# Performance work log

Measured on AMD Instinct MI355X. Metric: run time of the kernel, lower is better.

The kernel has to match this reference:

```python
import jax, jax.numpy as jnp
import numpy as np

B, T, DIM, S, DFF = 4, 2048, 2048, 4, 8192
SINKHORN_ITERS = 10


def setup_inputs() -> dict:
    key = jax.random.key(0)
    ks = jax.random.split(key, 12)

    def lin(k, fan_in, shape):
        bound = 1.0 / np.sqrt(fan_in)
        return jax.random.uniform(k, shape, jnp.float32, -bound, bound)

    return {
        "x": jax.random.normal(ks[0], (B, T, DIM), jnp.float32),
        # phi_* linears act on the S-times tiled vector of size S*DIM
        "phi_pre_w": lin(ks[1], S * DIM, (S, S * DIM)),
        "phi_pre_b": lin(ks[2], S * DIM, (S,)),
        "phi_post_w": lin(ks[3], S * DIM, (S, S * DIM)),
        "phi_post_b": lin(ks[4], S * DIM, (S,)),
        "phi_res_w": lin(ks[5], S * DIM, (S * S, S * DIM)),
        "phi_res_b": lin(ks[6], S * DIM, (S * S,)),
        "alpha_pre": jnp.ones((1,), jnp.float32),
        "alpha_post": jnp.ones((1,), jnp.float32),
        "alpha_res": jnp.ones((1,), jnp.float32),
        "b_pre": jnp.zeros((S,), jnp.float32),
        "b_post": jnp.zeros((S,), jnp.float32),
        "b_res": jnp.zeros((S, S), jnp.float32),
        # block = transformer MLP
        "W1": lin(ks[7], DIM, (DIM, DFF)),
        "b1": lin(ks[8], DIM, (DFF,)),
        "W2": lin(ks[9], DFF, (DFF, DIM)),
        "b2": lin(ks[10], DFF, (DIM,)),
    }


def sinkhorn_knopp(logits):
    # logits: [B, T, S, S] -> doubly-stochastic via exp + alternating normalization
    M = jnp.exp(logits)
    for _ in range(SINKHORN_ITERS):
        M = M / jnp.sum(M, axis=-1, keepdims=True)  # rows
        M = M / jnp.sum(M, axis=-2, keepdims=True)  # cols
    return M


def reference(x, phi_pre_w, phi_pre_b, phi_post_w, phi_post_b, phi_res_w,
              phi_res_b, alpha_pre, alpha_post, alpha_res, b_pre, b_post,
              b_res, W1, b1, W2, b2):
    bs, seq, d = x.shape
    s = b_pre.shape[0]
    eps = jnp.asarray(jnp.finfo(x.dtype).eps, x.dtype)
    # x_l = x expanded over S identical streams; x_vec = tile(x, S).
    # RMS over the tiled S*d vector == RMS over d (streams are copies).
    x_n = x * jax.lax.rsqrt(jnp.mean(x * x, axis=-1, keepdims=True) + eps)
    # Linear on the tiled vector == sum of the S weight blocks applied to x_n.
    Wp = phi_pre_w.reshape(s, s, d).sum(axis=1)        # [S, d]
    Wq = phi_post_w.reshape(s, s, d).sum(axis=1)       # [S, d]
    Wr = phi_res_w.reshape(s * s, s, d).sum(axis=1)    # [S*S, d]
    h_pre_t = alpha_pre * (jnp.einsum('btd,sd->bts', x_n, Wp) + phi_pre_b) + b_pre
    h_post_t = alpha_post * (jnp.einsum('btd,sd->bts', x_n, Wq) + phi_post_b) + b_post
    h_res_t = alpha_res * (jnp.einsum('btd,kd->btk', x_n, Wr) + phi_res_b)
    h_res_t = h_res_t.reshape(bs, seq, s, s) + b_res
    h_pre = jax.nn.sigmoid(h_pre_t)                    # [B,T,S]
    h_post = 2.0 * jax.nn.sigmoid(h_post_t)            # [B,T,S]
    h_res = sinkhorn_knopp(h_res_t)                    # [B,T,S,S]
    # block_input = sum_j x_l[:,:,j] * h_pre[...,j] ; streams identical -> x * sum_j h_pre
    block_input = x * jnp.sum(h_pre, axis=-1, keepdims=True)
    # block: MLP with exact (erf) GELU, matching torch default
    h = jax.nn.gelu(jnp.einsum('btd,df->btf', block_input, W1) + b1, approximate=False)
    block_out = jnp.einsum('btf,fd->btd', h, W2) + b2
    # out = sum_i [ (h_res @ x_l)_i + h_post_i * block_out ]
    #     = x * sum_{ij} h_res[ij] + block_out * sum_i h_post_i
    res_mix = jnp.sum(h_res, axis=(-2, -1))[..., None]         # [B,T,1]
    post_mix = jnp.sum(h_post, axis=-1, keepdims=True)          # [B,T,1]
    return x * res_mix + block_out * post_mix
```

## Files before the change

kernel.cpp:

```cpp
#include <hip/hip_runtime.h>
#include <hip/hip_bf16.h>
#include <cstdint>
#include <cstddef>

#define DIM   2048
#define DFF   8192
#define NROWS 8192
#define NFOLD 24

typedef float f32x4 __attribute__((ext_vector_type(4)));
typedef __bf16 bf16x8 __attribute__((ext_vector_type(8)));

__device__ __forceinline__ float sigmoidf_(float v) { return 1.0f / (1.0f + expf(-v)); }

__device__ __forceinline__ unsigned short f2bf(float v) {
    union { __hip_bfloat16 h; unsigned short u; } cv;
    cv.h = __float2bfloat16(v);
    return cv.u;
}

__device__ __forceinline__ void async_copy16(const void* g, void* l) {
    __builtin_amdgcn_global_load_lds((const __attribute__((address_space(1))) void*)g,
                                     (__attribute__((address_space(3))) void*)l, 16, 0, 0);
}

__device__ __forceinline__ void wg_barrier() {
    asm volatile("" ::: "memory");
    __builtin_amdgcn_s_barrier();
    asm volatile("" ::: "memory");
}

#define VM(n)  asm volatile("s_waitcnt vmcnt(" #n ")" ::: "memory")
#define LGKM0  asm volatile("s_waitcnt lgkmcnt(0)" ::: "memory")

__global__ __launch_bounds__(256) void fold_kernel(const float* __restrict__ pre_w,
                                                   const float* __restrict__ post_w,
                                                   const float* __restrict__ res_w,
                                                   float* __restrict__ Wfold) {
    int idx = blockIdx.x * 256 + threadIdx.x;
    if (idx >= NFOLD * DIM) return;
    int r = idx >> 11;
    int d = idx & (DIM - 1);
    const float* src;
    if (r < 4)      src = pre_w  + (size_t)r * (4 * DIM);
    else if (r < 8) src = post_w + (size_t)(r - 4) * (4 * DIM);
    else            src = res_w  + (size_t)(r - 8) * (4 * DIM);
    Wfold[idx] = src[d] + src[DIM + d] + src[2 * DIM + d] + src[3 * DIM + d];
}

__global__ __launch_bounds__(256) void transpose_to_bf16(const float* __restrict__ in,
                                                         __hip_bfloat16* __restrict__ out,
                                                         int R, int C) {
    __shared__ float tile[32][33];
    const int bx = blockIdx.x, by = blockIdx.y;
    const int t = threadIdx.x;
    const int lr = t >> 3;
    const int lc = (t & 7) * 4;

    float4 v = *(const float4*)(in + (size_t)(by * 32 + lr) * C + bx * 32 + lc);
    tile[lr][lc + 0] = v.x; tile[lr][lc + 1] = v.y;
    tile[lr][lc + 2] = v.z; tile[lr][lc + 3] = v.w;
    __syncthreads();

    ushort4 u;
    u.x = f2bf(tile[lc + 0][lr]); u.y = f2bf(tile[lc + 1][lr]);
    u.z = f2bf(tile[lc + 2][lr]); u.w = f2bf(tile[lc + 3][lr]);
    *reinterpret_cast<ushort4*>(out + (size_t)(bx * 32 + lr) * R + by * 32 + lc) = u;
}

__global__ __launch_bounds__(512) void gating_kernel(
    const float* __restrict__ x, const float* __restrict__ Wfold,
    const float* __restrict__ phi_pre_b, const float* __restrict__ phi_post_b,
    const float* __restrict__ phi_res_b,
    const float* __restrict__ alpha_pre, const float* __restrict__ alpha_post,
    const float* __restrict__ alpha_res,
    const float* __restrict__ b_pre, const float* __restrict__ b_post,
    const float* __restrict__ b_res,
    __hip_bfloat16* __restrict__ Abuf,
    float* __restrict__ g_res_arr, float* __restrict__ g_post_arr) {
    const int tid = threadIdx.x;
    const int lane = tid & 63, wave = tid >> 6;
    const int row = blockIdx.x * 8 + wave;

    const float4* x4 = (const float4*)x + (size_t)row * 512;
    const float4* w4 = (const float4*)Wfold;

    float4 xv[8];
#pragma unroll
    for (int j = 0; j < 8; j++) xv[j] = x4[j * 64 + lane];

    float p[25];
    p[24] = 0.f;
#pragma unroll
    for (int j = 0; j < 8; j++)
        p[24] += xv[j].x * xv[j].x + xv[j].y * xv[j].y + xv[j].z * xv[j].z + xv[j].w * xv[j].w;

    for (int r = 0; r < NFOLD; r++) {
        float acc = 0.f;
#pragma unroll
        for (int j = 0; j < 8; j++) {
            float4 wv = w4[r * 512 + j * 64 + lane];
            acc += xv[j].x * wv.x + xv[j].y * wv.y + xv[j].z * wv.z + xv[j].w * wv.w;
        }
        p[r] = acc;
    }

#pragma unroll
    for (int r = 0; r < 25; r++) {
        float v = p[r];
#pragma unroll
        for (int off = 1; off < 64; off <<= 1) v += __shfl_xor(v, off, 64);
        p[r] = v;
    }

    const float rms = rsqrtf(p[24] / (float)DIM + 1.1920928955078125e-07f);
    const float ap = alpha_pre[0], aq = alpha_post[0], ar = alpha_res[0];
    float gpre = 0.f, gpost = 0.f;
#pragma unroll
    for (int s = 0; s < 4; s++) {
        gpre  += sigmoidf_(ap * (rms * p[s]     + phi_pre_b[s])  + b_pre[s]);
        gpost += 2.0f * sigmoidf_(aq * (rms * p[4 + s] + phi_post_b[s]) + b_post[s]);
    }
    float Mm[4][4];
#pragma unroll
    for (int i = 0; i < 4; i++)
#pragma unroll
        for (int j = 0; j < 4; j++) {
            int k = i * 4 + j;
            Mm[i][j] = expf(ar * (rms * p[8 + k] + phi_res_b[k]) + b_res[k]);
        }
    for (int it = 0; it < 10; ++it) {
#pragma unroll
        for (int i = 0; i < 4; i++) {
            float rs = 1.0f / (Mm[i][0] + Mm[i][1] + Mm[i][2] + Mm[i][3]);
#pragma unroll
            for (int j = 0; j < 4; j++) Mm[i][j] *= rs;
        }
#pragma unroll
        for (int j = 0; j < 4; j++) {
            float cs = 1.0f / (Mm[0][j] + Mm[1][j] + Mm[2][j] + Mm[3][j]);
#pragma unroll
            for (int i = 0; i < 4; i++) Mm[i][j] *= cs;
        }
    }
    float gres = 0.f;
#pragma unroll
    for (int i = 0; i < 4; i++)
#pragma unroll
        for (int j = 0; j < 4; j++) gres += Mm[i][j];

    __hip_bfloat16* arow = Abuf + (size_t)row * DIM;
#pragma unroll
    for (int j = 0; j < 8; j++) {
        ushort4 u;
        u.x = f2bf(xv[j].x * gpre); u.y = f2bf(xv[j].y * gpre);
        u.z = f2bf(xv[j].z * gpre); u.w = f2bf(xv[j].w * gpre);
        *reinterpret_cast<ushort4*>(arow + (j * 64 + lane) * 4) = u;
    }
    if (lane == 0) {
        g_res_arr[row]  = gres;
        g_post_arr[row] = gpost;
    }
}

#define RD_A(DST, REG)                                                            \
    _Pragma("unroll") for (int m = 0; m < 4; ++m) {                               \
        DST[m][0] = *(const bf16x8*)((REG) + baseA + m * 2048 + cb0);             \
        DST[m][1] = *(const bf16x8*)((REG) + baseA + m * 2048 + cb1);             \
    }
#define RD_B(DST, REG)                                                            \
    _Pragma("unroll") for (int n = 0; n < 2; ++n) {                               \
        DST[n][0] = *(const bf16x8*)((REG) + baseB + n * 2048 + cb0);             \
        DST[n][1] = *(const bf16x8*)((REG) + baseB + n * 2048 + cb1);             \
    }

#define MQ(AF, BF, MO, NO)                                                        \
    __builtin_amdgcn_s_setprio(1);                                                \
    _Pragma("unroll") for (int m = 0; m < 4; ++m)                                 \
    _Pragma("unroll") for (int n = 0; n < 2; ++n) {                               \
        acc[(MO) + m][(NO) + n] = __builtin_amdgcn_mfma_f32_16x16x32_bf16(        \
            AF[m][0], BF[n][0], acc[(MO) + m][(NO) + n], 0, 0, 0);                \
        acc[(MO) + m][(NO) + n] = __builtin_amdgcn_mfma_f32_16x16x32_bf16(        \
            AF[m][1], BF[n][1], acc[(MO) + m][(NO) + n], 0, 0, 0);                \
    }                                                                             \
    __builtin_amdgcn_s_setprio(0);

#define STG_A(t_, h_)                                                             \
    if ((t_) < nk) {                                                              \
        char* l_ = ldsA + (((t_) & 1) * 32768) + (h_) * 16384 + wave * 1024;      \
        async_copy16(Ab + aOff[0][h_] + (size_t)(t_) * 128, l_);                  \
        async_copy16(Ab + aOff[1][h_] + (size_t)(t_) * 128, l_ + 8192);           \
    }
#define STG_B(t_, h_)                                                             \
    if ((t_) < nk) {                                                              \
        char* l_ = ldsB + (((t_) & 1) * 32768) + (h_) * 16384 + wave * 1024;      \
        async_copy16(Bb + bOff[0][h_] + (size_t)(t_) * 128, l_);                  \
        async_copy16(Bb + bOff[1][h_] + (size_t)(t_) * 128, l_ + 8192);           \
    }

template <int MODE, int NB, int PRE>
__global__ __launch_bounds__(512, 2) void gemm256(
    const __hip_bfloat16* __restrict__ A, const __hip_bfloat16* __restrict__ Bt,
    int M, int N, int K, const float* __restrict__ bias,
    __hip_bfloat16* __restrict__ outh, float* __restrict__ outf,
    const float* __restrict__ x, const float* __restrict__ g_res,
    const float* __restrict__ g_post) {
    __shared__ __align__(16) char ldsA[65536];
    __shared__ __align__(16) char ldsB[65536];

    const int wg = blockIdx.x;
    const int xcd = wg & 7;
    const int i = wg >> 3;
    const int nt = xcd * NB + (i % NB);
    const int mt = i / NB;
    const int m0 = mt * 256;
    const int n0 = nt * 256;

    const int tid = threadIdx.x;
    const int lane = tid & 63;
    const int wave = tid >> 6;
    const int wr = wave >> 2;
    const int wc = wave & 3;
    const int q = lane >> 4;
    const int rr = lane & 7;

    const uint32_t cb0 = (uint32_t)((q ^ rr) << 4);
    const uint32_t cb1 = (uint32_t)(((4 + q) ^ rr) << 4);
    const uint32_t baseA = (uint32_t)((wr * 64 + (lane & 15)) * 128);
    const uint32_t baseB = (uint32_t)((wc * 32 + (lane & 15)) * 128);

    const uint32_t scb = (uint32_t)((((lane & 7) ^ ((lane >> 3) & 7))) << 4);
    const int lr = lane >> 3;
    const size_t K2 = (size_t)K * 2;
    size_t aOff[2][2], bOff[2][2];
#pragma unroll
    for (int ii = 0; ii < 2; ++ii)
#pragma unroll
        for (int h = 0; h < 2; ++h) {
            int gA = m0 + wave * 8 + lr + ii * 128 + h * 64;
            int gB = n0 + ((wave >> 2) + 2 * ii) * 64 + h * 32 + (wave & 3) * 8 + lr;
            aOff[ii][h] = (size_t)gA * K2 + scb;
            bOff[ii][h] = (size_t)gB * K2 + scb;
        }
    const char* Ab = (const char*)A;
    const char* Bb = (const char*)Bt;

    f32x4 acc[8][4];
#pragma unroll
    for (int m = 0; m < 8; ++m)
#pragma unroll
        for (int n = 0; n < 4; ++n) acc[m][n] = (f32x4){0.f, 0.f, 0.f, 0.f};

    const int nk = K / 64;

    STG_A(0, 0); STG_B(0, 0); STG_B(0, 1); STG_A(0, 1);
    STG_A(1, 0); STG_B(1, 0);
    VM(4);
    wg_barrier();

    bf16x8 a0[4][2], a1[4][2];
    bf16x8 b0[2][2], b1[2][2];

    for (int kt = 0; kt < nk; ++kt) {
        const int c = kt & 1;
        const char* Ac = ldsA + c * 32768;
        const char* Bc = ldsB + c * 32768;
        RD_A(a0, Ac)
        RD_B(b0, Bc)
        RD_B(b1, Bc + 16384)
        STG_A(kt + 1, 1)
        STG_B(kt + 1, 1)
        if (PRE) { LGKM0; }
        wg_barrier();
        if (!PRE) { LGKM0; }
        MQ(a0, b0, 0, 0)
        MQ(a0, b1, 0, 2)
        RD_A(a1, Ac + 16384)
        STG_A(kt + 2, 0)
        STG_B(kt + 2, 0)
        if (PRE) { LGKM0; }
        if (kt + 2 < nk) { VM(4); } else { VM(0); }
        wg_barrier();
        if (!PRE) { LGKM0; }
        MQ(a1, b0, 4, 0)
        MQ(a1, b1, 4, 2)
    }

#pragma unroll
    for (int mi = 0; mi < 8; ++mi) {
#pragma unroll
        for (int ni = 0; ni < 4; ++ni) {
            const int col = n0 + wc * 64 + (ni >> 1) * 32 + (ni & 1) * 16 + (lane & 15);
            const float bc = bias[col];
#pragma unroll
            for (int j = 0; j < 4; ++j) {
                const int row = m0 + wr * 128 + (mi >> 2) * 64 + (mi & 3) * 16 + q * 4 + j;
                float v = acc[mi][ni][j] + bc;
                if (MODE == 1) {
                    float u = 1.5957691216057308f * (v + 0.044715f * v * v * v);
                    float s = 1.0f / (1.0f + __expf(-u));
                    outh[(size_t)row * N + col] = __float2bfloat16(v * s);
                } else {
                    outf[(size_t)row * N + col] =
                        x[(size_t)row * N + col] * g_res[row] + v * g_post[row];
                }
            }
        }
    }
}

extern "C" void kernel_launch(void* const* d_in, const int* in_sizes, int n_in,
                              void* d_out, int out_size, void* d_ws, size_t ws_size,
                              hipStream_t stream) {
    const float* x          = (const float*)d_in[0];
    const float* phi_pre_w  = (const float*)d_in[1];
    const float* phi_pre_b  = (const float*)d_in[2];
    const float* phi_post_w = (const float*)d_in[3];
    const float* phi_post_b = (const float*)d_in[4];
    const float* phi_res_w  = (const float*)d_in[5];
    const float* phi_res_b  = (const float*)d_in[6];
    const float* alpha_pre  = (const float*)d_in[7];
    const float* alpha_post = (const float*)d_in[8];
    const float* alpha_res  = (const float*)d_in[9];
    const float* b_pre      = (const float*)d_in[10];
    const float* b_post     = (const float*)d_in[11];
    const float* b_res      = (const float*)d_in[12];
    const float* W1         = (const float*)d_in[13];
    const float* b1         = (const float*)d_in[14];
    const float* W2         = (const float*)d_in[15];
    const float* b2         = (const float*)d_in[16];
    float* out = (float*)d_out;

    char* ws = (char*)d_ws;
    __hip_bfloat16* W1T  = (__hip_bfloat16*)ws;
    __hip_bfloat16* W2T  = W1T + (size_t)DFF * DIM;
    __hip_bfloat16* Abuf = W2T + (size_t)DIM * DFF;
    __hip_bfloat16* Hbuf = Abuf + (size_t)NROWS * DIM;
    float* Wfold = (float*)(Hbuf + (size_t)NROWS * DFF);
    float* gres  = Wfold + NFOLD * DIM;
    float* gpost = gres + NROWS;

    fold_kernel<<<(NFOLD * DIM + 255) / 256, 256, 0, stream>>>(phi_pre_w, phi_post_w,
                                                               phi_res_w, Wfold);
    transpose_to_bf16<<<dim3(DFF / 32, DIM / 32), 256, 0, stream>>>(W1, W1T, DIM, DFF);
    transpose_to_bf16<<<dim3(DIM / 32, DFF / 32), 256, 0, stream>>>(W2, W2T, DFF, DIM);
    gating_kernel<<<NROWS / 8, 512, 0, stream>>>(x, Wfold, phi_pre_b, phi_post_b, phi_res_b,
                                                 alpha_pre, alpha_post, alpha_res,
                                                 b_pre, b_post, b_res, Abuf, gres, gpost);
    gemm256<1, 4, 1><<<1024, 512, 0, stream>>>(
        Abuf, W1T, NROWS, DFF, DIM, b1, Hbuf, nullptr, nullptr, nullptr, nullptr);
    gemm256<2, 1, 0><<<256, 512, 0, stream>>>(
        Hbuf, W2T, NROWS, DIM, DFF, b2, nullptr, out, x, gres, gpost);
}
```

Measured before the change: 631.5 us.

## Use 32x32x16 MFMA tiles in the first MLP GEMM kernel

```diff
diff --git a/kernel.cpp b/kernel.cpp
--- a/kernel.cpp
+++ b/kernel.cpp
@@ -9,6 +9,7 @@
 #define NFOLD 24
 
 typedef float f32x4 __attribute__((ext_vector_type(4)));
+typedef float f32x16 __attribute__((ext_vector_type(16)));
 typedef __bf16 bf16x8 __attribute__((ext_vector_type(8)));
 
 __device__ __forceinline__ float sigmoidf_(float v) { return 1.0f / (1.0f + expf(-v)); }
@@ -163,6 +164,154 @@
     }
 }
 
+#define STG_A(t_, h_)                                                             \
+    if ((t_) < nk) {                                                              \
+        char* l_ = ldsA + (((t_) & 1) * 32768) + (h_) * 16384 + wave * 1024;      \
+        async_copy16(Ab + aOff[0][h_] + (size_t)(t_) * 128, l_);                  \
+        async_copy16(Ab + aOff[1][h_] + (size_t)(t_) * 128, l_ + 8192);           \
+    }
+#define STG_B(t_, h_)                                                             \
+    if ((t_) < nk) {                                                              \
+        char* l_ = ldsB + (((t_) & 1) * 32768) + (h_) * 16384 + wave * 1024;      \
+        async_copy16(Bb + bOff[0][h_] + (size_t)(t_) * 128, l_);                  \
+        async_copy16(Bb + bOff[1][h_] + (size_t)(t_) * 128, l_ + 8192);           \
+    }
+
+#define STAGE_ADDR_SETUP                                                          \
+    const uint32_t scb = (uint32_t)((((lane & 7) ^ ((lane >> 3) & 7))) << 4);     \
+    const int lr_ = lane >> 3;                                                    \
+    const size_t K2 = (size_t)K * 2;                                              \
+    size_t aOff[2][2], bOff[2][2];                                                \
+    _Pragma("unroll") for (int ii = 0; ii < 2; ++ii)                              \
+    _Pragma("unroll") for (int h = 0; h < 2; ++h) {                               \
+        int gA = m0 + wave * 8 + lr_ + ii * 128 + h * 64;                         \
+        int gB = n0 + ((wave >> 2) + 2 * ii) * 64 + h * 32 + (wave & 3) * 8 + lr_;\
+        aOff[ii][h] = (size_t)gA * K2 + scb;                                      \
+        bOff[ii][h] = (size_t)gB * K2 + scb;                                      \
+    }
+
+template <int NB>
+__global__ __launch_bounds__(512, 2) void gemm256_w32(
+    const __hip_bfloat16* __restrict__ A, const __hip_bfloat16* __restrict__ Bt,
+    int M, int N, int K, const float* __restrict__ bias,
+    __hip_bfloat16* __restrict__ outh) {
+    __shared__ __align__(16) char ldsA[65536];
+    __shared__ __align__(16) char ldsB[65536];
+
+    const int wg = blockIdx.x;
+    const int xcd = wg & 7;
+    const int i = wg >> 3;
+    const int nt = xcd * NB + (i % NB);
+    const int mt = i / NB;
+    const int m0 = mt * 256;
+    const int n0 = nt * 256;
+
+    const int tid = threadIdx.x;
+    const int lane = tid & 63;
+    const int wave = tid >> 6;
+    const int wr = wave >> 2;
+    const int wc = wave & 3;
+    const int lane31 = lane & 31;
+    const int lhalf = lane >> 5;
+    const int x7 = lane31 & 7;
+
+    uint32_t cb32[4];
+#pragma unroll
+    for (int ks = 0; ks < 4; ++ks)
+        cb32[ks] = (uint32_t)(((ks * 2 + lhalf) ^ x7) << 4);
+    const uint32_t bA0r = (uint32_t)((wr * 64 + lane31) * 128);
+    const uint32_t bA1r = (uint32_t)((wr * 64 + 32 + lane31) * 128);
+    const uint32_t bBr  = (uint32_t)((wc * 32 + lane31) * 128);
+
+    STAGE_ADDR_SETUP
+    const char* Ab = (const char*)A;
+    const char* Bb = (const char*)Bt;
+
+    f32x16 acc[4][2];
+#pragma unroll
+    for (int m = 0; m < 4; ++m)
+#pragma unroll
+        for (int n = 0; n < 2; ++n)
+#pragma unroll
+            for (int j = 0; j < 16; ++j) acc[m][n][j] = 0.f;
+
+    const int nk = K / 64;
+
+    STG_A(0, 0); STG_B(0, 0); STG_B(0, 1); STG_A(0, 1);
+    STG_A(1, 0); STG_B(1, 0);
+    VM(4);
+    wg_barrier();
+
+    bf16x8 fa[2][4], fa2[2][4], fb0[4], fb1[4];
+
+    for (int kt = 0; kt < nk; ++kt) {
+        const int c = kt & 1;
+        const char* Ac = ldsA + c * 32768;
+        const char* Bc = ldsB + c * 32768;
+#pragma unroll
+        for (int ks = 0; ks < 4; ++ks) {
+            fa[0][ks] = *(const bf16x8*)(Ac + bA0r + cb32[ks]);
+            fa[1][ks] = *(const bf16x8*)(Ac + bA1r + cb32[ks]);
+            fb0[ks]   = *(const bf16x8*)(Bc + bBr + cb32[ks]);
+            fb1[ks]   = *(const bf16x8*)(Bc + 16384 + bBr + cb32[ks]);
+        }
+        STG_A(kt + 1, 1)
+        STG_B(kt + 1, 1)
+        wg_barrier();
+        LGKM0;
+        __builtin_amdgcn_s_setprio(1);
+#pragma unroll
+        for (int m2 = 0; m2 < 2; ++m2)
+#pragma unroll
+            for (int ks = 0; ks < 4; ++ks) {
+                acc[m2][0] = __builtin_amdgcn_mfma_f32_32x32x16_bf16(
+                    fa[m2][ks], fb0[ks], acc[m2][0], 0, 0, 0);
+                acc[m2][1] = __builtin_amdgcn_mfma_f32_32x32x16_bf16(
+                    fa[m2][ks], fb1[ks], acc[m2][1], 0, 0, 0);
+            }
+        __builtin_amdgcn_s_setprio(0);
+#pragma unroll
+        for (int ks = 0; ks < 4; ++ks) {
+            fa2[0][ks] = *(const bf16x8*)(Ac + 16384 + bA0r + cb32[ks]);
+            fa2[1][ks] = *(const bf16x8*)(Ac + 16384 + bA1r + cb32[ks]);
+        }
+        STG_A(kt + 2, 0)
+        STG_B(kt + 2, 0)
+        if (kt + 2 < nk) { VM(4); } else { VM(0); }
+        wg_barrier();
+        LGKM0;
+        __builtin_amdgcn_s_setprio(1);
+#pragma unroll
+        for (int m2 = 0; m2 < 2; ++m2)
+#pragma unroll
+            for (int ks = 0; ks < 4; ++ks) {
+                acc[2 + m2][0] = __builtin_amdgcn_mfma_f32_32x32x16_bf16(
+                    fa2[m2][ks], fb0[ks], acc[2 + m2][0], 0, 0, 0);
+                acc[2 + m2][1] = __builtin_amdgcn_mfma_f32_32x32x16_bf16(
+                    fa2[m2][ks], fb1[ks], acc[2 + m2][1], 0, 0, 0);
+            }
+        __builtin_amdgcn_s_setprio(0);
+    }
+
+#pragma unroll
+    for (int mi = 0; mi < 4; ++mi) {
+#pragma unroll
+        for (int ni = 0; ni < 2; ++ni) {
+            const int col = n0 + wc * 64 + ni * 32 + lane31;
+            const float bc = bias[col];
+            const int rb = m0 + wr * 128 + (mi >> 1) * 64 + (mi & 1) * 32 + 4 * lhalf;
+#pragma unroll
+            for (int reg = 0; reg < 16; ++reg) {
+                const int row = rb + (reg & 3) + 8 * (reg >> 2);
+                float v = acc[mi][ni][reg] + bc;
+                float u = 1.5957691216057308f * (v + 0.044715f * v * v * v);
+                float s = 1.0f / (1.0f + __expf(-u));
+                outh[(size_t)row * N + col] = __float2bfloat16(v * s);
+            }
+        }
+    }
+}
+
 #define RD_A(DST, REG)                                                            \
     _Pragma("unroll") for (int m = 0; m < 4; ++m) {                               \
         DST[m][0] = *(const bf16x8*)((REG) + baseA + m * 2048 + cb0);             \
@@ -185,20 +334,7 @@
     }                                                                             \
     __builtin_amdgcn_s_setprio(0);
 
-#define STG_A(t_, h_)                                                             \
-    if ((t_) < nk) {                                                              \
-        char* l_ = ldsA + (((t_) & 1) * 32768) + (h_) * 16384 + wave * 1024;      \
-        async_copy16(Ab + aOff[0][h_] + (size_t)(t_) * 128, l_);                  \
-        async_copy16(Ab + aOff[1][h_] + (size_t)(t_) * 128, l_ + 8192);           \
-    }
-#define STG_B(t_, h_)                                                             \
-    if ((t_) < nk) {                                                              \
-        char* l_ = ldsB + (((t_) & 1) * 32768) + (h_) * 16384 + wave * 1024;      \
-        async_copy16(Bb + bOff[0][h_] + (size_t)(t_) * 128, l_);                  \
-        async_copy16(Bb + bOff[1][h_] + (size_t)(t_) * 128, l_ + 8192);           \
-    }
-
-template <int MODE, int NB, int PRE>
+template <int MODE, int NB>
 __global__ __launch_bounds__(512, 2) void gemm256(
     const __hip_bfloat16* __restrict__ A, const __hip_bfloat16* __restrict__ Bt,
     int M, int N, int K, const float* __restrict__ bias,
@@ -229,19 +365,7 @@
     const uint32_t baseA = (uint32_t)((wr * 64 + (lane & 15)) * 128);
     const uint32_t baseB = (uint32_t)((wc * 32 + (lane & 15)) * 128);
 
-    const uint32_t scb = (uint32_t)((((lane & 7) ^ ((lane >> 3) & 7))) << 4);
-    const int lr = lane >> 3;
-    const size_t K2 = (size_t)K * 2;
-    size_t aOff[2][2], bOff[2][2];
-#pragma unroll
-    for (int ii = 0; ii < 2; ++ii)
-#pragma unroll
-        for (int h = 0; h < 2; ++h) {
-            int gA = m0 + wave * 8 + lr + ii * 128 + h * 64;
-            int gB = n0 + ((wave >> 2) + 2 * ii) * 64 + h * 32 + (wave & 3) * 8 + lr;
-            aOff[ii][h] = (size_t)gA * K2 + scb;
-            bOff[ii][h] = (size_t)gB * K2 + scb;
-        }
+    STAGE_ADDR_SETUP
     const char* Ab = (const char*)A;
     const char* Bb = (const char*)Bt;
 
@@ -270,18 +394,16 @@
         RD_B(b1, Bc + 16384)
         STG_A(kt + 1, 1)
         STG_B(kt + 1, 1)
-        if (PRE) { LGKM0; }
         wg_barrier();
-        if (!PRE) { LGKM0; }
+        LGKM0;
         MQ(a0, b0, 0, 0)
         MQ(a0, b1, 0, 2)
         RD_A(a1, Ac + 16384)
         STG_A(kt + 2, 0)
         STG_B(kt + 2, 0)
-        if (PRE) { LGKM0; }
         if (kt + 2 < nk) { VM(4); } else { VM(0); }
         wg_barrier();
-        if (!PRE) { LGKM0; }
+        LGKM0;
         MQ(a1, b0, 4, 0)
         MQ(a1, b1, 4, 2)
     }
@@ -347,8 +469,8 @@
     gating_kernel<<<NROWS / 8, 512, 0, stream>>>(x, Wfold, phi_pre_b, phi_post_b, phi_res_b,
                                                  alpha_pre, alpha_post, alpha_res,
                                                  b_pre, b_post, b_res, Abuf, gres, gpost);
-    gemm256<1, 4, 1><<<1024, 512, 0, stream>>>(
-        Abuf, W1T, NROWS, DFF, DIM, b1, Hbuf, nullptr, nullptr, nullptr, nullptr);
-    gemm256<2, 1, 0><<<256, 512, 0, stream>>>(
+    gemm256_w32<4><<<1024, 512, 0, stream>>>(
+        Abuf, W1T, NROWS, DFF, DIM, b1, Hbuf);
+    gemm256<2, 1><<<256, 512, 0, stream>>>(
         Hbuf, W2T, NROWS, DIM, DFF, b2, nullptr, out, x, gres, gpost);
 }
```

New measurement: 661.7 us. 4.8% more time.
